# Kernel tuning notes

Hardware: AMD Instinct MI355X
Metric: run time of the kernel (lower is better)

## Reference

```python
import jax, jax.numpy as jnp
import numpy as np

N_NODES = 100000
N_EDGES = 1600000
IN_FEAT = 64
HIDDEN = 128
N_CLASSES = 16
N_GRAPHS = 512


def _glorot(key, shape):
    fan_in, fan_out = shape
    lim = (6.0 / (fan_in + fan_out)) ** 0.5
    return jax.random.uniform(key, shape, jnp.float32, -lim, lim)


def setup_inputs() -> dict:
    key = jax.random.key(0)
    ks = jax.random.split(key, 12)
    x = jax.random.normal(ks[0], (N_NODES, IN_FEAT), jnp.float32)
    edge_index = jax.random.randint(ks[1], (2, N_EDGES), 0, N_NODES, jnp.int64)
    batch = jnp.sort(jax.random.randint(ks[2], (N_NODES,), 0, N_GRAPHS, jnp.int64))
    # SAGEConv params: lin_l (neighbor agg, with bias), lin_r (root, no bias)
    params = {}
    dims = [(IN_FEAT, HIDDEN), (HIDDEN, HIDDEN), (HIDDEN, HIDDEN)]
    for i, (din, dout) in enumerate(dims, start=1):
        params[f"Wl{i}"] = _glorot(ks[2 + 2 * i - 1], (din, dout))
        params[f"bl{i}"] = jnp.zeros((dout,), jnp.float32)
        params[f"Wr{i}"] = _glorot(ks[2 + 2 * i], (din, dout))
    params["W_out"] = _glorot(ks[9], (HIDDEN, N_CLASSES))
    params["b_out"] = jnp.zeros((N_CLASSES,), jnp.float32)
    return {"x": x, "edge_index": edge_index, "batch": batch, **params}


def _sage_conv(x, src, dst, Wl, bl, Wr):
    # mean aggregation of neighbor (source) features onto target nodes
    msg = x[src]                                                # [E, D]
    agg_sum = jax.ops.segment_sum(msg, dst, num_segments=N_NODES)
    cnt = jax.ops.segment_sum(jnp.ones((src.shape[0],), x.dtype), dst,
                              num_segments=N_NODES)
    agg = agg_sum / jnp.maximum(cnt, 1.0)[:, None]
    return agg @ Wl + bl + x @ Wr


def reference(x, edge_index, batch, Wl1, bl1, Wr1, Wl2, bl2, Wr2,
              Wl3, bl3, Wr3, W_out, b_out):
    src, dst = edge_index[0], edge_index[1]
    h = jax.nn.relu(_sage_conv(x, src, dst, Wl1, bl1, Wr1))
    h = jax.nn.relu(_sage_conv(h, src, dst, Wl2, bl2, Wr2))
    h = _sage_conv(h, src, dst, Wl3, bl3, Wr3)
    # global mean pool over graphs
    g_sum = jax.ops.segment_sum(h, batch, num_segments=N_GRAPHS)
    g_cnt = jax.ops.segment_sum(jnp.ones((h.shape[0],), h.dtype), batch,
                                num_segments=N_GRAPHS)
    g = g_sum / jnp.maximum(g_cnt, 1.0)[:, None]
    # dropout is identity at inference (module.eval())
    return g @ W_out + b_out
```

## Files before the change

kernel.cpp:

```cpp
#include <hip/hip_runtime.h>

#define N_NODES   100000
#define N_PAD     100096
#define N_EDGES   1600000
#define IN_FEAT   64
#define HIDDEN    128
#define N_CLASSES 16
#define N_GRAPHS  512
#define MAXDEG    64
#define PSEG      12

#define BIN_NODES 512
#define NBINS     196
#define N_NODES_B (NBINS * BIN_NODES)
#define BINCAP    9000
#define EPB       2048

#define CONVBLK   3128
#define PACKBLK   192

typedef __attribute__((ext_vector_type(8))) unsigned short us8;
typedef __attribute__((ext_vector_type(8))) short s8v;
typedef __attribute__((ext_vector_type(4))) float f4v;

__device__ __forceinline__ unsigned short f2bf(float f) {
    unsigned u = __builtin_bit_cast(unsigned, f);
    unsigned r = u + 0x7FFFu + ((u >> 16) & 1u);
    return (unsigned short)(r >> 16);
}
__device__ __forceinline__ float bf2f(unsigned short h) {
    unsigned u = ((unsigned)h) << 16;
    return __builtin_bit_cast(float, u);
}
__device__ __forceinline__ void acc8(float* a, us8 v) {
#pragma unroll
    for (int e = 0; e < 8; e++) a[e] += bf2f(v[e]);
}


__global__ __launch_bounds__(512) void bin_kernel(const int* __restrict__ src,
                                                  const int* __restrict__ dst,
                                                  int* __restrict__ bin_cursor,
                                                  int2* __restrict__ binbuf) {
    __shared__ int hist[NBINS];
    __shared__ int base[NBINS];
    const int t = threadIdx.x;
    for (int i = t; i < NBINS; i += 512) hist[i] = 0;
    __syncthreads();

    const int e0 = blockIdx.x * EPB;
    int myb[4], mys[4], myd[4], myp[4];
#pragma unroll
    for (int j = 0; j < 4; j++) {
        int e = e0 + t + j * 512;
        if (e < N_EDGES) {
            myd[j] = dst[e];
            mys[j] = src[e];
            myb[j] = myd[j] >> 9;
        } else {
            myb[j] = -1; mys[j] = 0; myd[j] = 0;
        }
    }
#pragma unroll
    for (int j = 0; j < 4; j++)
        myp[j] = (myb[j] >= 0) ? atomicAdd(&hist[myb[j]], 1) : 0;
    __syncthreads();

    for (int i = t; i < NBINS; i += 512) {
        int h = hist[i];
        base[i] = (h > 0) ? atomicAdd(&bin_cursor[i], h) : 0;
    }
    __syncthreads();

#pragma unroll
    for (int j = 0; j < 4; j++) {
        if (myb[j] >= 0) {
            int pos = base[myb[j]] + myp[j];
            if (pos < BINCAP)
                binbuf[(size_t)myb[j] * BINCAP + pos] = make_int2(mys[j], myd[j]);
        }
    }
}


__global__ __launch_bounds__(512) void build_kernel(const int2* __restrict__ binbuf,
                                                    const int* __restrict__ bin_cursor,
                                                    int* __restrict__ cursor,
                                                    int* __restrict__ csr) {
    __shared__ int lcur[BIN_NODES];
    __shared__ int lcsr[BIN_NODES * MAXDEG];
    const int b = blockIdx.x, t = threadIdx.x;
    if (t < BIN_NODES) lcur[t] = 0;
    __syncthreads();

    int cnt = bin_cursor[b];
    if (cnt > BINCAP) cnt = BINCAP;
    const int2* __restrict__ eb = binbuf + (size_t)b * BINCAP;
    for (int i = t; i < cnt; i += 512) {
        int2 e = eb[i];
        int dl = e.y - b * BIN_NODES;
        int p = atomicAdd(&lcur[dl], 1);
        if (p < MAXDEG) lcsr[dl * MAXDEG + p] = e.x;
    }
    __syncthreads();

    int4* __restrict__ gout = reinterpret_cast<int4*>(csr + (size_t)b * BIN_NODES * MAXDEG);
    const int4* __restrict__ lin = reinterpret_cast<const int4*>(lcsr);
    for (int i = t; i < BIN_NODES * MAXDEG / 4; i += 512) gout[i] = lin[i];
    if (t < BIN_NODES) cursor[b * BIN_NODES + t] = lcur[t];
}


__global__ __launch_bounds__(256) void prep_kernel(
        const float* __restrict__ x, ushort* __restrict__ xh,
        const float* __restrict__ s0, const float* __restrict__ s1,
        const float* __restrict__ s2, const float* __restrict__ s3,
        ushort* __restrict__ Bpk) {
    if (blockIdx.x < CONVBLK) {
        const int flat = blockIdx.x * 256 + threadIdx.x;
        const int row = flat >> 3;
        us8 w;
        if (row < N_NODES) {
            const float* p = x + (size_t)flat * 8;
            float4 v0 = *reinterpret_cast<const float4*>(p);
            float4 v1 = *reinterpret_cast<const float4*>(p + 4);
            w[0] = f2bf(v0.x); w[1] = f2bf(v0.y); w[2] = f2bf(v0.z); w[3] = f2bf(v0.w);
            w[4] = f2bf(v1.x); w[5] = f2bf(v1.y); w[6] = f2bf(v1.z); w[7] = f2bf(v1.w);
        } else {
#pragma unroll
            for (int e = 0; e < 8; e++) w[e] = 0;
        }
        reinterpret_cast<us8*>(xh)[flat] = w;
    } else {
        const int flat = (blockIdx.x - CONVBLK) * 256 + threadIdx.x;
        const float* src; int base;
        if      (flat < 8192)  { src = s0; base = 0; }
        else if (flat < 16384) { src = s1; base = 8192; }
        else if (flat < 32768) { src = s2; base = 16384; }
        else                   { src = s3; base = 32768; }
        const int local = flat - base;
        const int j    = local & 7;
        const int lane = (local >> 3) & 63;
        const int tile = local >> 9;
        const int ks = tile >> 3, ct = tile & 7;
        const int row = ks * 32 + ((lane >> 4) << 3) + j;
        const int col = (ct << 4) + (lane & 15);
        Bpk[flat] = f2bf(src[row * 128 + col]);
    }
}


template <int D>
__global__ __launch_bounds__(256, 4) void aggregate_bf(
        const ushort* __restrict__ feat, const int* __restrict__ cursor,
        const int* __restrict__ csr, ushort* __restrict__ aggout) {
    constexpr int LPN = D / 8;
    constexpr int NPB = 256 / LPN;
    const int tid  = threadIdx.x;
    const int lane = tid & (LPN - 1);
    const int n    = blockIdx.x * NPB + tid / LPN;
    if (n >= N_NODES) return;
    const int start = n * MAXDEG;
    int cnt = cursor[n];
    if (cnt > MAXDEG) cnt = MAXDEG;
    const us8* __restrict__ f8 = reinterpret_cast<const us8*>(feat);

    float a[8] = {0.f, 0.f, 0.f, 0.f, 0.f, 0.f, 0.f, 0.f};
    int i = 0;
    for (; i + 16 <= cnt; i += 16) {
        int t[16];
#pragma unroll
        for (int u = 0; u < 16; u++) t[u] = csr[start + i + u];
        us8 v[16];
#pragma unroll
        for (int u = 0; u < 16; u++) v[u] = f8[(size_t)t[u] * LPN + lane];
#pragma unroll
        for (int u = 0; u < 16; u++) acc8(a, v[u]);
    }
    for (; i + 8 <= cnt; i += 8) {
        int t[8];
#pragma unroll
        for (int u = 0; u < 8; u++) t[u] = csr[start + i + u];
        us8 v[8];
#pragma unroll
        for (int u = 0; u < 8; u++) v[u] = f8[(size_t)t[u] * LPN + lane];
#pragma unroll
        for (int u = 0; u < 8; u++) acc8(a, v[u]);
    }
    for (; i + 4 <= cnt; i += 4) {
        int t0 = csr[start + i + 0], t1 = csr[start + i + 1];
        int t2 = csr[start + i + 2], t3 = csr[start + i + 3];
        us8 v0 = f8[(size_t)t0 * LPN + lane];
        us8 v1 = f8[(size_t)t1 * LPN + lane];
        us8 v2 = f8[(size_t)t2 * LPN + lane];
        us8 v3 = f8[(size_t)t3 * LPN + lane];
        acc8(a, v0); acc8(a, v1); acc8(a, v2); acc8(a, v3);
    }
    for (; i < cnt; i++) {
        us8 v0 = f8[(size_t)csr[start + i] * LPN + lane];
        acc8(a, v0);
    }
    const float inv = 1.f / (float)(cnt > 0 ? cnt : 1);
    us8 w;
#pragma unroll
    for (int e = 0; e < 8; e++) w[e] = f2bf(a[e] * inv);
    reinterpret_cast<us8*>(aggout)[(size_t)n * LPN + lane] = w;
}


template <int K, bool RELU>
__global__ __launch_bounds__(256, 2) void gemm_mfma(
        const ushort* __restrict__ A1, const ushort* __restrict__ A2,
        const ushort* __restrict__ B1p, const ushort* __restrict__ B2p,
        const float* __restrict__ bias, ushort* __restrict__ out) {
    constexpr int KS = K / 32;
    __shared__ ushort Bs[2 * KS * 8 * 512];
    const int tid = threadIdx.x;
    {
        const us8* g1 = reinterpret_cast<const us8*>(B1p);
        const us8* g2 = reinterpret_cast<const us8*>(B2p);
        us8* l8 = reinterpret_cast<us8*>(Bs);
        constexpr int PH = KS * 512;
#pragma unroll
        for (int i = 0; i < 4 * KS; i++) {
            int c = i * 256 + tid;
            if (i < 2 * KS) l8[c] = g1[c];
            else            l8[c] = g2[c - PH];
        }
    }
    __syncthreads();

    const int wave = tid >> 6, lane = tid & 63;
    const int r0 = blockIdx.x * 128 + wave * 32;
    const size_t arow = (size_t)(r0 + (lane & 15));
    const int koff = (lane >> 4) << 3;

    f4v acc[2][8];
#pragma unroll
    for (int rt = 0; rt < 2; rt++)
#pragma unroll
        for (int ct = 0; ct < 8; ct++) acc[rt][ct] = (f4v){0.f, 0.f, 0.f, 0.f};

    const s8v* Bf = reinterpret_cast<const s8v*>(Bs);
#pragma unroll
    for (int ph = 0; ph < 2; ph++) {
        const ushort* __restrict__ A = ph ? A2 : A1;
#pragma unroll
        for (int ks = 0; ks < KS; ks++) {
            s8v a0 = *reinterpret_cast<const s8v*>(A + arow * K + ks * 32 + koff);
            s8v a1 = *reinterpret_cast<const s8v*>(A + (arow + 16) * K + ks * 32 + koff);
#pragma unroll
            for (int ct = 0; ct < 8; ct++) {
                s8v b = Bf[((ph * KS + ks) * 8 + ct) * 64 + lane];
                acc[0][ct] = __builtin_amdgcn_mfma_f32_16x16x32_bf16(a0, b, acc[0][ct], 0, 0, 0);
                acc[1][ct] = __builtin_amdgcn_mfma_f32_16x16x32_bf16(a1, b, acc[1][ct], 0, 0, 0);
            }
        }
    }

    const int colb = lane & 15;
    const int rowb = (lane >> 4) << 2;
#pragma unroll
    for (int rt = 0; rt < 2; rt++) {
#pragma unroll
        for (int ct = 0; ct < 8; ct++) {
            const int col = ct * 16 + colb;
            const float bb = bias[col];
#pragma unroll
            for (int j = 0; j < 4; j++) {
                int row = r0 + rt * 16 + rowb + j;
                if (row < N_NODES) {
                    float v = acc[rt][ct][j] + bb;
                    if (RELU) v = fmaxf(v, 0.f);
                    out[(size_t)row * HIDDEN + col] = f2bf(v);
                }
            }
        }
    }
}


__global__ __launch_bounds__(256) void edge_pool(
        const ushort* __restrict__ h2, const int* __restrict__ batch,
        const int* __restrict__ cursor, const int* __restrict__ csr,
        float* __restrict__ Pe, float* __restrict__ Pn, int* __restrict__ gcnt) {
    const int blk = blockIdx.x;
    const int gid = blk / PSEG, seg = blk % PSEG;
    __shared__ int sb[2];
    __shared__ float red[4][2][128];
    const int tid = threadIdx.x;
    if (tid < 2) {
        int target = gid + tid;
        int lo = 0, hi = N_NODES;
        while (lo < hi) {
            int mid = (lo + hi) >> 1;
            if (batch[mid] < target) lo = mid + 1; else hi = mid;
        }
        sb[tid] = lo;
    }
    __syncthreads();
    const int s = sb[0], e = sb[1], len = e - s;
    const int per = (len + PSEG - 1) / PSEG;
    const int ss = s + seg * per;
    int ee = ss + per; if (ee > e) ee = e;

    const int ch  = tid & 15;
    const int grp = tid >> 4;
    const us8* __restrict__ f8 = reinterpret_cast<const us8*>(h2);
    float pe[8] = {0.f, 0.f, 0.f, 0.f, 0.f, 0.f, 0.f, 0.f};
    float pn[8] = {0.f, 0.f, 0.f, 0.f, 0.f, 0.f, 0.f, 0.f};

    for (int n = ss + grp; n < ee; n += 16) {
        const int start = n * MAXDEG;
        int cnt = cursor[n];
        if (cnt > MAXDEG) cnt = MAXDEG;
        float a[8] = {0.f, 0.f, 0.f, 0.f, 0.f, 0.f, 0.f, 0.f};
        int i = 0;
        for (; i + 8 <= cnt; i += 8) {
            int t0 = csr[start + i + 0], t1 = csr[start + i + 1];
            int t2 = csr[start + i + 2], t3 = csr[start + i + 3];
            int t4 = csr[start + i + 4], t5 = csr[start + i + 5];
            int t6 = csr[start + i + 6], t7 = csr[start + i + 7];
            us8 v0 = f8[(size_t)t0 * 16 + ch];
            us8 v1 = f8[(size_t)t1 * 16 + ch];
            us8 v2 = f8[(size_t)t2 * 16 + ch];
            us8 v3 = f8[(size_t)t3 * 16 + ch];
            us8 v4 = f8[(size_t)t4 * 16 + ch];
            us8 v5 = f8[(size_t)t5 * 16 + ch];
            us8 v6 = f8[(size_t)t6 * 16 + ch];
            us8 v7 = f8[(size_t)t7 * 16 + ch];
            acc8(a, v0); acc8(a, v1); acc8(a, v2); acc8(a, v3);
            acc8(a, v4); acc8(a, v5); acc8(a, v6); acc8(a, v7);
        }
        for (; i + 4 <= cnt; i += 4) {
            int t0 = csr[start + i + 0], t1 = csr[start + i + 1];
            int t2 = csr[start + i + 2], t3 = csr[start + i + 3];
            us8 v0 = f8[(size_t)t0 * 16 + ch];
            us8 v1 = f8[(size_t)t1 * 16 + ch];
            us8 v2 = f8[(size_t)t2 * 16 + ch];
            us8 v3 = f8[(size_t)t3 * 16 + ch];
            acc8(a, v0); acc8(a, v1); acc8(a, v2); acc8(a, v3);
        }
        for (; i < cnt; i++) {
            us8 v0 = f8[(size_t)csr[start + i] * 16 + ch];
            acc8(a, v0);
        }
        const float inv = 1.f / (float)(cnt > 0 ? cnt : 1);
#pragma unroll
        for (int j = 0; j < 8; j++) pe[j] += a[j] * inv;
        us8 v = f8[(size_t)n * 16 + ch];
        acc8(pn, v);
    }

#pragma unroll
    for (int j = 0; j < 8; j++) {
        pe[j] += __shfl_xor(pe[j], 16); pe[j] += __shfl_xor(pe[j], 32);
        pn[j] += __shfl_xor(pn[j], 16); pn[j] += __shfl_xor(pn[j], 32);
    }
    const int wave = tid >> 6, lane = tid & 63;
    if (lane < 16) {
#pragma unroll
        for (int j = 0; j < 8; j++) {
            red[wave][0][lane * 8 + j] = pe[j];
            red[wave][1][lane * 8 + j] = pn[j];
        }
    }
    __syncthreads();
    if (tid < 128) {
        float se = red[0][0][tid] + red[1][0][tid] + red[2][0][tid] + red[3][0][tid];
        float sn = red[0][1][tid] + red[1][1][tid] + red[2][1][tid] + red[3][1][tid];
        Pe[(size_t)blk * 128 + tid] = se;
        Pn[(size_t)blk * 128 + tid] = sn;
    }
    if (tid == 0 && seg == 0) gcnt[gid] = len;
}


__global__ __launch_bounds__(128) void head_fused(
        const float* __restrict__ Pe, const float* __restrict__ Pn,
        const int* __restrict__ gcnt,
        const float* __restrict__ Wl3, const float* __restrict__ Wr3,
        const float* __restrict__ bl3,
        const float* __restrict__ Wout, const float* __restrict__ bout,
        float* __restrict__ out) {
    const int gid = blockIdx.x, c = threadIdx.x;
    __shared__ float lse[128], lsn[128], lg[128];
    float se = 0.f, sn = 0.f;
#pragma unroll
    for (int sg = 0; sg < PSEG; sg++) {
        se += Pe[(size_t)(gid * PSEG + sg) * 128 + c];
        sn += Pn[(size_t)(gid * PSEG + sg) * 128 + c];
    }
    const int len = gcnt[gid];
    const float inv = 1.f / (float)(len > 0 ? len : 1);
    lse[c] = se * inv;
    lsn[c] = sn * inv;
    __syncthreads();
    float acc = (len > 0) ? bl3[c] : 0.f;
    for (int k = 0; k < 128; k++)
        acc += lse[k] * Wl3[k * 128 + c] + lsn[k] * Wr3[k * 128 + c];
    lg[c] = acc;
    __syncthreads();
    if (c < N_CLASSES) {
        float o = bout[c];
        for (int k = 0; k < 128; k++) o += lg[k] * Wout[k * N_CLASSES + c];
        out[(size_t)gid * N_CLASSES + c] = o;
    }
}


extern "C" void kernel_launch(void* const* d_in, const int* in_sizes, int n_in,
                              void* d_out, int out_size, void* d_ws, size_t ws_size,
                              hipStream_t stream) {
    const float* x    = (const float*)d_in[0];
    const int* eidx   = (const int*)d_in[1];
    const int* batch  = (const int*)d_in[2];
    const float* Wl1  = (const float*)d_in[3];
    const float* bl1  = (const float*)d_in[4];
    const float* Wr1  = (const float*)d_in[5];
    const float* Wl2  = (const float*)d_in[6];
    const float* bl2  = (const float*)d_in[7];
    const float* Wr2  = (const float*)d_in[8];
    const float* Wl3  = (const float*)d_in[9];
    const float* bl3  = (const float*)d_in[10];
    const float* Wr3  = (const float*)d_in[11];
    const float* Wout = (const float*)d_in[12];
    const float* bout = (const float*)d_in[13];
    float* out = (float*)d_out;

    const int* esrc = eidx;
    const int* edst = eidx + N_EDGES;

    char* ws = (char*)d_ws;
    size_t o = 0;
    int*  bin_cursor = (int*)(ws + o);  o += 256 * 4;
    int*  cursor     = (int*)(ws + o);  o += (size_t)N_NODES_B * 4;
    int*  csr        = (int*)(ws + o);  o += (size_t)N_NODES_B * MAXDEG * 4;
    int2* binbuf     = (int2*)(ws + o); o += (size_t)NBINS * BINCAP * 8;
    o = (o + 255) & ~(size_t)255;
    ushort* xh   = (ushort*)(ws + o); o += (size_t)N_PAD * IN_FEAT * 2;
    ushort* aggb = (ushort*)(ws + o); o += (size_t)N_PAD * HIDDEN * 2;
    ushort* h1b  = (ushort*)(ws + o); o += (size_t)N_PAD * HIDDEN * 2;
    ushort* h2b  = (ushort*)(ws + o); o += (size_t)N_PAD * HIDDEN * 2;
    ushort* Bpk  = (ushort*)(ws + o); o += (size_t)49152 * 2;
    float*  Pe   = (float*)(ws + o);  o += (size_t)N_GRAPHS * PSEG * 128 * 4;
    float*  Pn   = (float*)(ws + o);  o += (size_t)N_GRAPHS * PSEG * 128 * 4;
    int*    gcnt = (int*)(ws + o);    o += (size_t)N_GRAPHS * 4;

    hipMemsetAsync(bin_cursor, 0, 256 * 4, stream);

    bin_kernel<<<(N_EDGES + EPB - 1) / EPB, 512, 0, stream>>>(esrc, edst, bin_cursor, binbuf);
    build_kernel<<<NBINS, 512, 0, stream>>>(binbuf, bin_cursor, cursor, csr);

    prep_kernel<<<CONVBLK + PACKBLK, 256, 0, stream>>>(x, xh, Wl1, Wr1, Wl2, Wr2, Bpk);

    ushort* Wl1p = Bpk + 0,     *Wr1p = Bpk + 8192;
    ushort* Wl2p = Bpk + 16384, *Wr2p = Bpk + 32768;

    const int GB = N_PAD / 128;

    aggregate_bf<IN_FEAT><<<(N_NODES + 31) / 32, 256, 0, stream>>>(xh, cursor, csr, aggb);
    gemm_mfma<IN_FEAT, true><<<GB, 256, 0, stream>>>(aggb, xh, Wl1p, Wr1p, bl1, h1b);
    aggregate_bf<HIDDEN><<<(N_NODES + 15) / 16, 256, 0, stream>>>(h1b, cursor, csr, aggb);
    gemm_mfma<HIDDEN, true><<<GB, 256, 0, stream>>>(aggb, h1b, Wl2p, Wr2p, bl2, h2b);
    edge_pool<<<N_GRAPHS * PSEG, 256, 0, stream>>>(h2b, batch, cursor, csr, Pe, Pn, gcnt);
    head_fused<<<N_GRAPHS, 128, 0, stream>>>(Pe, Pn, gcnt, Wl3, Wr3, bl3, Wout, bout, out);
}
```

Measured before the change: 383.1 us.

## Replace per-graph segmented edge pool with per-node blocks and atomic graph accumulation

The final pooling kernel now runs one block per 16 nodes instead of a fixed 12 segments per graph. Each block reduces its nodes by graph id in shared memory and atomically adds into per-graph sums, which are zeroed by a new memset. The graph size is now found by binary search in the head kernel. The 16-way unrolled path in the aggregation kernel is also dropped, leaving 8-way as the widest unroll. The intent is better load balance and occupancy for the pooling stage, paid for with float atomics, which make the summation order nondeterministic.

```diff
diff --git a/kernel.cpp b/kernel.cpp
--- a/kernel.cpp
+++ b/kernel.cpp
@@ -8,7 +8,6 @@
 #define N_CLASSES 16
 #define N_GRAPHS  512
 #define MAXDEG    64
-#define PSEG      12
 
 #define BIN_NODES 512
 #define NBINS     196
@@ -167,16 +166,6 @@
 
     float a[8] = {0.f, 0.f, 0.f, 0.f, 0.f, 0.f, 0.f, 0.f};
     int i = 0;
-    for (; i + 16 <= cnt; i += 16) {
-        int t[16];
-#pragma unroll
-        for (int u = 0; u < 16; u++) t[u] = csr[start + i + u];
-        us8 v[16];
-#pragma unroll
-        for (int u = 0; u < 16; u++) v[u] = f8[(size_t)t[u] * LPN + lane];
-#pragma unroll
-        for (int u = 0; u < 16; u++) acc8(a, v[u]);
-    }
     for (; i + 8 <= cnt; i += 8) {
         int t[8];
 #pragma unroll
@@ -280,121 +269,104 @@
 }
 
 
-__global__ __launch_bounds__(256) void edge_pool(
+__global__ __launch_bounds__(256, 4) void epool(
         const ushort* __restrict__ h2, const int* __restrict__ batch,
         const int* __restrict__ cursor, const int* __restrict__ csr,
-        float* __restrict__ Pe, float* __restrict__ Pn, int* __restrict__ gcnt) {
-    const int blk = blockIdx.x;
-    const int gid = blk / PSEG, seg = blk % PSEG;
-    __shared__ int sb[2];
-    __shared__ float red[4][2][128];
+        float* __restrict__ Pe, float* __restrict__ Pn) {
+    __shared__ float red[16][2][128];
+    __shared__ int sgid[16];
     const int tid = threadIdx.x;
-    if (tid < 2) {
-        int target = gid + tid;
-        int lo = 0, hi = N_NODES;
-        while (lo < hi) {
-            int mid = (lo + hi) >> 1;
-            if (batch[mid] < target) lo = mid + 1; else hi = mid;
-        }
-        sb[tid] = lo;
-    }
-    __syncthreads();
-    const int s = sb[0], e = sb[1], len = e - s;
-    const int per = (len + PSEG - 1) / PSEG;
-    const int ss = s + seg * per;
-    int ee = ss + per; if (ee > e) ee = e;
-
-    const int ch  = tid & 15;
-    const int grp = tid >> 4;
+    const int ch = tid & 15, grp = tid >> 4;
+    const int n = blockIdx.x * 16 + grp;
+    const int gid = batch[n];
+    if (ch == 0) sgid[grp] = gid;
+
+    const int start = n * MAXDEG;
+    int cnt = cursor[n];
+    if (cnt > MAXDEG) cnt = MAXDEG;
     const us8* __restrict__ f8 = reinterpret_cast<const us8*>(h2);
-    float pe[8] = {0.f, 0.f, 0.f, 0.f, 0.f, 0.f, 0.f, 0.f};
-    float pn[8] = {0.f, 0.f, 0.f, 0.f, 0.f, 0.f, 0.f, 0.f};
-
-    for (int n = ss + grp; n < ee; n += 16) {
-        const int start = n * MAXDEG;
-        int cnt = cursor[n];
-        if (cnt > MAXDEG) cnt = MAXDEG;
-        float a[8] = {0.f, 0.f, 0.f, 0.f, 0.f, 0.f, 0.f, 0.f};
-        int i = 0;
-        for (; i + 8 <= cnt; i += 8) {
-            int t0 = csr[start + i + 0], t1 = csr[start + i + 1];
-            int t2 = csr[start + i + 2], t3 = csr[start + i + 3];
-            int t4 = csr[start + i + 4], t5 = csr[start + i + 5];
-            int t6 = csr[start + i + 6], t7 = csr[start + i + 7];
-            us8 v0 = f8[(size_t)t0 * 16 + ch];
-            us8 v1 = f8[(size_t)t1 * 16 + ch];
-            us8 v2 = f8[(size_t)t2 * 16 + ch];
-            us8 v3 = f8[(size_t)t3 * 16 + ch];
-            us8 v4 = f8[(size_t)t4 * 16 + ch];
-            us8 v5 = f8[(size_t)t5 * 16 + ch];
-            us8 v6 = f8[(size_t)t6 * 16 + ch];
-            us8 v7 = f8[(size_t)t7 * 16 + ch];
-            acc8(a, v0); acc8(a, v1); acc8(a, v2); acc8(a, v3);
-            acc8(a, v4); acc8(a, v5); acc8(a, v6); acc8(a, v7);
-        }
-        for (; i + 4 <= cnt; i += 4) {
-            int t0 = csr[start + i + 0], t1 = csr[start + i + 1];
-            int t2 = csr[start + i + 2], t3 = csr[start + i + 3];
-            us8 v0 = f8[(size_t)t0 * 16 + ch];
-            us8 v1 = f8[(size_t)t1 * 16 + ch];
-            us8 v2 = f8[(size_t)t2 * 16 + ch];
-            us8 v3 = f8[(size_t)t3 * 16 + ch];
-            acc8(a, v0); acc8(a, v1); acc8(a, v2); acc8(a, v3);
-        }
-        for (; i < cnt; i++) {
-            us8 v0 = f8[(size_t)csr[start + i] * 16 + ch];
-            acc8(a, v0);
-        }
-        const float inv = 1.f / (float)(cnt > 0 ? cnt : 1);
-#pragma unroll
-        for (int j = 0; j < 8; j++) pe[j] += a[j] * inv;
-        us8 v = f8[(size_t)n * 16 + ch];
-        acc8(pn, v);
-    }
-
+
+    float a[8] = {0.f, 0.f, 0.f, 0.f, 0.f, 0.f, 0.f, 0.f};
+    int i = 0;
+    for (; i + 8 <= cnt; i += 8) {
+        int t0 = csr[start + i + 0], t1 = csr[start + i + 1];
+        int t2 = csr[start + i + 2], t3 = csr[start + i + 3];
+        int t4 = csr[start + i + 4], t5 = csr[start + i + 5];
+        int t6 = csr[start + i + 6], t7 = csr[start + i + 7];
+        us8 v0 = f8[(size_t)t0 * 16 + ch];
+        us8 v1 = f8[(size_t)t1 * 16 + ch];
+        us8 v2 = f8[(size_t)t2 * 16 + ch];
+        us8 v3 = f8[(size_t)t3 * 16 + ch];
+        us8 v4 = f8[(size_t)t4 * 16 + ch];
+        us8 v5 = f8[(size_t)t5 * 16 + ch];
+        us8 v6 = f8[(size_t)t6 * 16 + ch];
+        us8 v7 = f8[(size_t)t7 * 16 + ch];
+        acc8(a, v0); acc8(a, v1); acc8(a, v2); acc8(a, v3);
+        acc8(a, v4); acc8(a, v5); acc8(a, v6); acc8(a, v7);
+    }
+    for (; i + 4 <= cnt; i += 4) {
+        int t0 = csr[start + i + 0], t1 = csr[start + i + 1];
+        int t2 = csr[start + i + 2], t3 = csr[start + i + 3];
+        us8 v0 = f8[(size_t)t0 * 16 + ch];
+        us8 v1 = f8[(size_t)t1 * 16 + ch];
+        us8 v2 = f8[(size_t)t2 * 16 + ch];
+        us8 v3 = f8[(size_t)t3 * 16 + ch];
+        acc8(a, v0); acc8(a, v1); acc8(a, v2); acc8(a, v3);
+    }
+    for (; i < cnt; i++) {
+        us8 v0 = f8[(size_t)csr[start + i] * 16 + ch];
+        acc8(a, v0);
+    }
+    const float inv = 1.f / (float)(cnt > 0 ? cnt : 1);
+    us8 self = f8[(size_t)n * 16 + ch];
 #pragma unroll
     for (int j = 0; j < 8; j++) {
-        pe[j] += __shfl_xor(pe[j], 16); pe[j] += __shfl_xor(pe[j], 32);
-        pn[j] += __shfl_xor(pn[j], 16); pn[j] += __shfl_xor(pn[j], 32);
-    }
-    const int wave = tid >> 6, lane = tid & 63;
-    if (lane < 16) {
-#pragma unroll
-        for (int j = 0; j < 8; j++) {
-            red[wave][0][lane * 8 + j] = pe[j];
-            red[wave][1][lane * 8 + j] = pn[j];
-        }
-    }
-    __syncthreads();
+        red[grp][0][ch * 8 + j] = a[j] * inv;
+        red[grp][1][ch * 8 + j] = bf2f(self[j]);
+    }
+    __syncthreads();
+
+    const int gfirst = sgid[0], glast = sgid[15];
     if (tid < 128) {
-        float se = red[0][0][tid] + red[1][0][tid] + red[2][0][tid] + red[3][0][tid];
-        float sn = red[0][1][tid] + red[1][1][tid] + red[2][1][tid] + red[3][1][tid];
-        Pe[(size_t)blk * 128 + tid] = se;
-        Pn[(size_t)blk * 128 + tid] = sn;
-    }
-    if (tid == 0 && seg == 0) gcnt[gid] = len;
+        for (int g = gfirst; g <= glast; ++g) {
+            float se = 0.f, sn = 0.f;
+#pragma unroll
+            for (int k = 0; k < 16; k++) {
+                bool m = (sgid[k] == g);
+                se += m ? red[k][0][tid] : 0.f;
+                sn += m ? red[k][1][tid] : 0.f;
+            }
+            atomicAdd(&Pe[(size_t)g * 128 + tid], se);
+            atomicAdd(&Pn[(size_t)g * 128 + tid], sn);
+        }
+    }
 }
 
 
 __global__ __launch_bounds__(128) void head_fused(
         const float* __restrict__ Pe, const float* __restrict__ Pn,
-        const int* __restrict__ gcnt,
+        const int* __restrict__ batch,
         const float* __restrict__ Wl3, const float* __restrict__ Wr3,
         const float* __restrict__ bl3,
         const float* __restrict__ Wout, const float* __restrict__ bout,
         float* __restrict__ out) {
     const int gid = blockIdx.x, c = threadIdx.x;
     __shared__ float lse[128], lsn[128], lg[128];
-    float se = 0.f, sn = 0.f;
-#pragma unroll
-    for (int sg = 0; sg < PSEG; sg++) {
-        se += Pe[(size_t)(gid * PSEG + sg) * 128 + c];
-        sn += Pn[(size_t)(gid * PSEG + sg) * 128 + c];
-    }
-    const int len = gcnt[gid];
+    __shared__ int sb[2];
+    if (c < 2) {
+        int target = gid + c;
+        int lo = 0, hi = N_NODES;
+        while (lo < hi) {
+            int mid = (lo + hi) >> 1;
+            if (batch[mid] < target) lo = mid + 1; else hi = mid;
+        }
+        sb[c] = lo;
+    }
+    __syncthreads();
+    const int len = sb[1] - sb[0];
     const float inv = 1.f / (float)(len > 0 ? len : 1);
-    lse[c] = se * inv;
-    lsn[c] = sn * inv;
+    lse[c] = Pe[(size_t)gid * 128 + c] * inv;
+    lsn[c] = Pn[(size_t)gid * 128 + c] * inv;
     __syncthreads();
     float acc = (len > 0) ? bl3[c] : 0.f;
     for (int k = 0; k < 128; k++)
@@ -443,11 +415,12 @@
     ushort* h1b  = (ushort*)(ws + o); o += (size_t)N_PAD * HIDDEN * 2;
     ushort* h2b  = (ushort*)(ws + o); o += (size_t)N_PAD * HIDDEN * 2;
     ushort* Bpk  = (ushort*)(ws + o); o += (size_t)49152 * 2;
-    float*  Pe   = (float*)(ws + o);  o += (size_t)N_GRAPHS * PSEG * 128 * 4;
-    float*  Pn   = (float*)(ws + o);  o += (size_t)N_GRAPHS * PSEG * 128 * 4;
-    int*    gcnt = (int*)(ws + o);    o += (size_t)N_GRAPHS * 4;
+    o = (o + 255) & ~(size_t)255;
+    float*  Pe   = (float*)(ws + o);  o += (size_t)N_GRAPHS * 128 * 4;
+    float*  Pn   = (float*)(ws + o);  o += (size_t)N_GRAPHS * 128 * 4;
 
     hipMemsetAsync(bin_cursor, 0, 256 * 4, stream);
+    hipMemsetAsync(Pe, 0, (size_t)N_GRAPHS * 128 * 4 * 2, stream);
 
     bin_kernel<<<(N_EDGES + EPB - 1) / EPB, 512, 0, stream>>>(esrc, edst, bin_cursor, binbuf);
     build_kernel<<<NBINS, 512, 0, stream>>>(binbuf, bin_cursor, cursor, csr);
@@ -463,6 +436,6 @@
     gemm_mfma<IN_FEAT, true><<<GB, 256, 0, stream>>>(aggb, xh, Wl1p, Wr1p, bl1, h1b);
     aggregate_bf<HIDDEN><<<(N_NODES + 15) / 16, 256, 0, stream>>>(h1b, cursor, csr, aggb);
     gemm_mfma<HIDDEN, true><<<GB, 256, 0, stream>>>(aggb, h1b, Wl2p, Wr2p, bl2, h2b);
-    edge_pool<<<N_GRAPHS * PSEG, 256, 0, stream>>>(h2b, batch, cursor, csr, Pe, Pn, gcnt);
-    head_fused<<<N_GRAPHS, 128, 0, stream>>>(Pe, Pn, gcnt, Wl3, Wr3, bl3, Wout, bout, out);
-}
+    epool<<<N_NODES / 16, 256, 0, stream>>>(h2b, batch, cursor, csr, Pe, Pn);
+    head_fused<<<N_GRAPHS, 128, 0, stream>>>(Pe, Pn, batch, Wl3, Wr3, bl3, Wout, bout, out);
+}
```

Measured after the change: 353.2 us. 7.8% less time.
